# Optimization experiments

Hardware: AMD Instinct MI355X
Metric: run time of the kernel (lower is better)

## Reference

```python
import jax, jax.numpy as jnp
import numpy as np

N_NODES = 100000
N_EDGES = 3200000
IN_DIM, HID_DIM, LAT_DIM = 128, 64, 64


def gcn_conv(x, edge_index, W, b):
    """PyG-style GCNConv: add self-loops, symmetric deg^-1/2 normalization,
    linear transform, scatter-add aggregation, bias."""
    N = x.shape[0]
    loops = jnp.arange(N, dtype=edge_index.dtype)
    src = jnp.concatenate([edge_index[0], loops])  # [E+N]
    dst = jnp.concatenate([edge_index[1], loops])  # [E+N]
    # degree on target index (with self loops)
    deg = jax.ops.segment_sum(jnp.ones_like(dst, dtype=x.dtype), dst, num_segments=N)
    dinv = jnp.where(deg > 0, jax.lax.rsqrt(deg), 0.0)
    norm = dinv[src] * dinv[dst]  # [E+N]
    h = x @ W  # [N, out_dim] -- transform BEFORE gather (out_dim <= in_dim)
    msg = h[src] * norm[:, None]  # [E+N, out_dim]
    out = jax.ops.segment_sum(msg, dst, num_segments=N)
    return out + b


def setup_inputs() -> dict:
    key = jax.random.key(0)
    ks = jax.random.split(key, 6)
    x = jax.random.normal(ks[0], (N_NODES, IN_DIM), dtype=jnp.float32)
    edge_index = jax.random.randint(ks[1], (2, N_EDGES), 0, N_NODES, dtype=jnp.int64)
    # Glorot-ish init for weights, zero bias (PyG default)
    W1 = jax.random.normal(ks[2], (IN_DIM, HID_DIM), dtype=jnp.float32) / np.sqrt(IN_DIM)
    b1 = jnp.zeros((HID_DIM,), dtype=jnp.float32)
    W2 = jax.random.normal(ks[3], (HID_DIM, LAT_DIM), dtype=jnp.float32) / np.sqrt(HID_DIM)
    b2 = jnp.zeros((LAT_DIM,), dtype=jnp.float32)
    return {"x": x, "edge_index": edge_index, "W1": W1, "b1": b1, "W2": W2, "b2": b2}


def reference(x, edge_index, W1, b1, W2, b2):
    h = jax.nn.relu(gcn_conv(x, edge_index, W1, b1))
    return gcn_conv(h, edge_index, W2, b2)
```

## Files before the change

kernel.cpp:

```cpp
#include <hip/hip_runtime.h>
#include <cstdint>


#define BSHIFT 7
#define NBMAX 784
#define CH 4096
#define MAXB 6016

typedef __attribute__((ext_vector_type(8))) short bf16x8;
typedef __attribute__((ext_vector_type(4))) float f32x4;

__device__ inline unsigned short f2bf(float f) {
    unsigned u = __float_as_uint(f);
    unsigned r = (u + 0x7FFFu + ((u >> 16) & 1u)) >> 16;
    return (unsigned short)r;
}
__device__ inline unsigned pack2(float a, float b) {
    return (unsigned)f2bf(a) | ((unsigned)f2bf(b) << 16);
}
__device__ inline float blo(unsigned u) { return __uint_as_float(u << 16); }
__device__ inline float bhi(unsigned u) { return __uint_as_float(u & 0xFFFF0000u); }

__global__ __launch_bounds__(256) void hist_kernel(const int* __restrict__ dst,
                                                   int* __restrict__ histmat,
                                                   int E, int nb, int nblk,
                                                   const float* __restrict__ W1,
                                                   const float* __restrict__ W2,
                                                   unsigned short* __restrict__ W1t,
                                                   unsigned short* __restrict__ W2t) {
    if (blockIdx.x >= (unsigned)nblk) {
        int i = (blockIdx.x - nblk) * 256 + threadIdx.x;
        if (i < 128 * 64) {
            int k = i >> 6, n = i & 63;
            W1t[n * 128 + k] = f2bf(W1[i]);
        }
        int j = i - 128 * 64;
        if (j >= 0 && j < 64 * 64) {
            int k = j >> 6, n = j & 63;
            W2t[n * 64 + k] = f2bf(W2[j]);
        }
        return;
    }
    __shared__ int hist[NBMAX];
    int t = threadIdx.x;
    for (int b = t; b < nb; b += 256) hist[b] = 0;
    __syncthreads();
    int base = blockIdx.x * CH;
#pragma unroll
    for (int j = 0; j < CH / 1024; ++j) {
        int idx = base + j * 1024 + t * 4;
        if (idx + 4 <= E) {
            int4 d = *(const int4*)(dst + idx);
            atomicAdd(&hist[d.x >> BSHIFT], 1);
            atomicAdd(&hist[d.y >> BSHIFT], 1);
            atomicAdd(&hist[d.z >> BSHIFT], 1);
            atomicAdd(&hist[d.w >> BSHIFT], 1);
        } else {
            for (int k = 0; k < 4; ++k)
                if (idx + k < E) atomicAdd(&hist[dst[idx + k] >> BSHIFT], 1);
        }
    }
    __syncthreads();
    for (int b = t; b < nb; b += 256) histmat[blockIdx.x * nb + b] = hist[b];
}

__global__ __launch_bounds__(256) void scancol_kernel(const int* __restrict__ histmat,
                                                      int* __restrict__ colbase,
                                                      int* __restrict__ buckettotal,
                                                      int nb, int nblk) {
    __shared__ int ts[256];
    int b = blockIdx.x;
    int t = threadIdx.x;
    int v[4];
    int tsum = 0;
#pragma unroll
    for (int k = 0; k < 4; ++k) {
        int blk = t * 4 + k;
        v[k] = (blk < nblk) ? histmat[blk * nb + b] : 0;
        tsum += v[k];
    }
    ts[t] = tsum;
    __syncthreads();
    for (int ofs = 1; ofs < 256; ofs <<= 1) {
        int val = (t >= ofs) ? ts[t - ofs] : 0;
        __syncthreads();
        ts[t] += val;
        __syncthreads();
    }
    int run = ts[t] - tsum;
#pragma unroll
    for (int k = 0; k < 4; ++k) {
        int blk = t * 4 + k;
        if (blk < nblk) colbase[blk * nb + b] = run;
        run += v[k];
    }
    if (t == 255) buckettotal[b] = ts[255];
}

__global__ __launch_bounds__(256) void scanbucket_kernel(const int* __restrict__ buckettotal,
                                                         int* __restrict__ bucketbase,
                                                         int nb, int E) {
    __shared__ int ts[256];
    int t = threadIdx.x;
    int v[4];
    int tsum = 0;
#pragma unroll
    for (int k = 0; k < 4; ++k) {
        int b = t * 4 + k;
        v[k] = (b < nb) ? buckettotal[b] : 0;
        tsum += v[k];
    }
    ts[t] = tsum;
    __syncthreads();
    for (int ofs = 1; ofs < 256; ofs <<= 1) {
        int val = (t >= ofs) ? ts[t - ofs] : 0;
        __syncthreads();
        ts[t] += val;
        __syncthreads();
    }
    int run = ts[t] - tsum;
#pragma unroll
    for (int k = 0; k < 4; ++k) {
        int b = t * 4 + k;
        if (b < nb) bucketbase[b] = run;
        run += v[k];
    }
    if (t == 0) bucketbase[nb] = E;
}

__global__ __launch_bounds__(256) void bscatter_kernel(const int* __restrict__ src,
                                                       const int* __restrict__ dst,
                                                       const int* __restrict__ colbase,
                                                       const int* __restrict__ bucketbase,
                                                       int* __restrict__ packed,
                                                       int E, int nb) {
    __shared__ int cur[NBMAX];
    int t = threadIdx.x;
    for (int b = t; b < nb; b += 256)
        cur[b] = bucketbase[b] + colbase[blockIdx.x * nb + b];
    __syncthreads();
    int base = blockIdx.x * CH;
#pragma unroll
    for (int j = 0; j < CH / 1024; ++j) {
        int idx = base + j * 1024 + t * 4;
        if (idx + 4 <= E) {
            int4 d = *(const int4*)(dst + idx);
            int4 s = *(const int4*)(src + idx);
            int p;
            p = atomicAdd(&cur[d.x >> BSHIFT], 1); packed[p] = ((d.x & 127) << 17) | s.x;
            p = atomicAdd(&cur[d.y >> BSHIFT], 1); packed[p] = ((d.y & 127) << 17) | s.y;
            p = atomicAdd(&cur[d.z >> BSHIFT], 1); packed[p] = ((d.z & 127) << 17) | s.z;
            p = atomicAdd(&cur[d.w >> BSHIFT], 1); packed[p] = ((d.w & 127) << 17) | s.w;
        } else {
            for (int k = 0; k < 4; ++k)
                if (idx + k < E) {
                    int dd = dst[idx + k], ss = src[idx + k];
                    int p = atomicAdd(&cur[dd >> BSHIFT], 1);
                    packed[p] = ((dd & 127) << 17) | ss;
                }
        }
    }
}

__global__ __launch_bounds__(256) void bcsr_kernel(const int* __restrict__ packed,
                                                   const int* __restrict__ bucketbase,
                                                   int* __restrict__ rowptr,
                                                   float* __restrict__ dinv,
                                                   int* __restrict__ csr,
                                                   int N, int nb) {
    __shared__ int deg[128];
    __shared__ int lrp[128];
    __shared__ int ts[128];
    __shared__ int ebuf[MAXB];
    __shared__ int obuf[MAXB];
    int b = blockIdx.x;
    int t = threadIdx.x;
    if (t < 128) deg[t] = 0;
    __syncthreads();
    int bb0 = bucketbase[b];
    int bb1 = bucketbase[b + 1];
    int cnt = bb1 - bb0;
    bool fits = (cnt <= MAXB);
    if (fits) {
        for (int i = t; i < cnt; i += 256) {
            int v = packed[bb0 + i];
            ebuf[i] = v;
            atomicAdd(&deg[v >> 17], 1);
        }
    } else {
        for (int i = t; i < cnt; i += 256)
            atomicAdd(&deg[packed[bb0 + i] >> 17], 1);
    }
    __syncthreads();
    if (t < 128) ts[t] = deg[t];
    __syncthreads();
    for (int ofs = 1; ofs < 128; ofs <<= 1) {
        int v = (t < 128 && t >= ofs) ? ts[t - ofs] : 0;
        __syncthreads();
        if (t < 128) ts[t] += v;
        __syncthreads();
    }
    int node0 = b << BSHIFT;
    int nlocal = min(128, N - node0);
    if (t < 128) lrp[t] = ts[t] - deg[t];
    if (t < nlocal) {
        rowptr[node0 + t] = bb0 + (ts[t] - deg[t]);
        dinv[node0 + t] = rsqrtf((float)(deg[t] + 1));
    }
    if (t == nlocal) rowptr[node0 + nlocal] = bb1;
    __syncthreads();
    if (fits) {
        for (int i = t; i < cnt; i += 256) {
            int v = ebuf[i];
            int p = atomicAdd(&lrp[v >> 17], 1);
            obuf[p] = v & 0x1FFFF;
        }
        __syncthreads();
        for (int i = t; i < cnt; i += 256) csr[bb0 + i] = obuf[i];
    } else {
        for (int i = t; i < cnt; i += 256) {
            int v = packed[bb0 + i];
            int p = atomicAdd(&lrp[v >> 17], 1);
            csr[bb0 + p] = v & 0x1FFFF;
        }
    }
}

template <int K, bool XBF16>
__global__ __launch_bounds__(256) void gemm_mfma(const void* __restrict__ Xv,
                                                 const unsigned short* __restrict__ Wt,
                                                 const float* __restrict__ dinv,
                                                 unsigned short* __restrict__ Ybf, int M) {
    constexpr int KP = K + 8;
    __shared__ unsigned short Xs[64 * KP];
    __shared__ unsigned short Ws[64 * KP];
    int t = threadIdx.x;
    int row0 = blockIdx.x * 64;

    for (int i = t; i < 64 * K / 8; i += 256) {
        int r = i / (K / 8), c8 = i % (K / 8);
        *(uint4*)(&Ws[r * KP + c8 * 8]) = ((const uint4*)Wt)[i];
    }
    if (XBF16) {
        const unsigned short* X = (const unsigned short*)Xv;
        for (int i = t; i < 64 * K / 8; i += 256) {
            int r = i / (K / 8), c8 = i % (K / 8);
            int gr = row0 + r;
            uint4 v = make_uint4(0u, 0u, 0u, 0u);
            if (gr < M) v = ((const uint4*)(X + (size_t)gr * K))[c8];
            *(uint4*)(&Xs[r * KP + c8 * 8]) = v;
        }
    } else {
        const float* X = (const float*)Xv;
        for (int i = t; i < 64 * K / 4; i += 256) {
            int r = i / (K / 4), c4 = i % (K / 4);
            int gr = row0 + r;
            float4 v = make_float4(0.f, 0.f, 0.f, 0.f);
            if (gr < M) v = ((const float4*)(X + (size_t)gr * K))[c4];
            uint2 p;
            p.x = pack2(v.x, v.y);
            p.y = pack2(v.z, v.w);
            *(uint2*)(&Xs[r * KP + c4 * 4]) = p;
        }
    }
    __syncthreads();

    int lane = t & 63;
    int w = t >> 6;
    int m = lane & 15;
    int q = lane >> 4;

    f32x4 acc[4];
#pragma unroll
    for (int nt = 0; nt < 4; ++nt) acc[nt] = (f32x4){0.f, 0.f, 0.f, 0.f};

#pragma unroll
    for (int s = 0; s < K / 32; ++s) {
        bf16x8 a = *(const bf16x8*)(&Xs[(16 * w + m) * KP + s * 32 + q * 8]);
#pragma unroll
        for (int nt = 0; nt < 4; ++nt) {
            bf16x8 b = *(const bf16x8*)(&Ws[(16 * nt + m) * KP + s * 32 + q * 8]);
            acc[nt] = __builtin_amdgcn_mfma_f32_16x16x32_bf16(a, b, acc[nt], 0, 0, 0);
        }
    }
    __syncthreads();

    unsigned short* Cs = Xs;
#pragma unroll
    for (int nt = 0; nt < 4; ++nt)
#pragma unroll
        for (int r = 0; r < 4; ++r) {
            int row = 16 * w + q * 4 + r;
            int gr = row0 + row;
            float d = (gr < M) ? dinv[gr] : 0.f;
            Cs[row * 72 + nt * 16 + m] = f2bf(acc[nt][r] * d);
        }
    __syncthreads();
    for (int i = t; i < 64 * 64 / 8; i += 256) {
        int r = i >> 3, c8 = i & 7;
        int gr = row0 + r;
        if (gr < M)
            *(uint4*)(Ybf + (size_t)gr * 64 + c8 * 8) = *(const uint4*)(&Cs[r * 72 + c8 * 8]);
    }
}

__global__ __launch_bounds__(256) void aggregate_kernel(const unsigned* __restrict__ hsu,
                                                        const int* __restrict__ rowptr,
                                                        const int* __restrict__ csr,
                                                        const float* __restrict__ dinv,
                                                        const float* __restrict__ bias,
                                                        void* __restrict__ outv, int N,
                                                        int do_relu, int obf) {
    int t = threadIdx.x;
    int node = blockIdx.x * 32 + (t >> 3);
    if (node >= N) return;
    int sub = t & 7;
    int gbase = t & 56;

    float acc[8];
    {
        uint4 v = *(const uint4*)(hsu + (size_t)node * 32 + sub * 4);
        acc[0] = blo(v.x); acc[1] = bhi(v.x);
        acc[2] = blo(v.y); acc[3] = bhi(v.y);
        acc[4] = blo(v.z); acc[5] = bhi(v.z);
        acc[6] = blo(v.w); acc[7] = bhi(v.w);
    }
    int e0 = rowptr[node];
    int e1 = rowptr[node + 1];

    int e = e0;
    for (; e + 8 <= e1; e += 8) {
        int idx = csr[e + sub];
#pragma unroll
        for (int j = 0; j < 8; ++j) {
            int s = __shfl(idx, gbase + j, 64);
            uint4 v = *(const uint4*)(hsu + (size_t)s * 32 + sub * 4);
            acc[0] += blo(v.x); acc[1] += bhi(v.x);
            acc[2] += blo(v.y); acc[3] += bhi(v.y);
            acc[4] += blo(v.z); acc[5] += bhi(v.z);
            acc[6] += blo(v.w); acc[7] += bhi(v.w);
        }
    }
    for (; e < e1; ++e) {
        int s = csr[e];
        uint4 v = *(const uint4*)(hsu + (size_t)s * 32 + sub * 4);
        acc[0] += blo(v.x); acc[1] += bhi(v.x);
        acc[2] += blo(v.y); acc[3] += bhi(v.y);
        acc[4] += blo(v.z); acc[5] += bhi(v.z);
        acc[6] += blo(v.w); acc[7] += bhi(v.w);
    }

    float d = dinv[node];
    float4 b0 = *(const float4*)(bias + sub * 8);
    float4 b1 = *(const float4*)(bias + sub * 8 + 4);
    float o[8];
    o[0] = fmaf(acc[0], d, b0.x); o[1] = fmaf(acc[1], d, b0.y);
    o[2] = fmaf(acc[2], d, b0.z); o[3] = fmaf(acc[3], d, b0.w);
    o[4] = fmaf(acc[4], d, b1.x); o[5] = fmaf(acc[5], d, b1.y);
    o[6] = fmaf(acc[6], d, b1.z); o[7] = fmaf(acc[7], d, b1.w);
    if (do_relu) {
#pragma unroll
        for (int k = 0; k < 8; ++k) o[k] = fmaxf(o[k], 0.f);
    }
    if (obf) {
        unsigned short* outb = (unsigned short*)outv;
        uint4 p;
        p.x = pack2(o[0], o[1]); p.y = pack2(o[2], o[3]);
        p.z = pack2(o[4], o[5]); p.w = pack2(o[6], o[7]);
        *(uint4*)(outb + (size_t)node * 64 + sub * 8) = p;
    } else {
        float* op = (float*)outv + (size_t)node * 64 + sub * 8;
        *(float4*)(op)     = make_float4(o[0], o[1], o[2], o[3]);
        *(float4*)(op + 4) = make_float4(o[4], o[5], o[6], o[7]);
    }
}

extern "C" void kernel_launch(void* const* d_in, const int* in_sizes, int n_in,
                              void* d_out, int out_size, void* d_ws, size_t ws_size,
                              hipStream_t stream) {
    const float* x  = (const float*)d_in[0];
    const int*   ei = (const int*)d_in[1];
    const float* W1 = (const float*)d_in[2];
    const float* b1 = (const float*)d_in[3];
    const float* W2 = (const float*)d_in[4];
    const float* b2 = (const float*)d_in[5];

    const int N = in_sizes[0] / 128;
    const int E = in_sizes[1] / 2;
    const int* src = ei;
    const int* dst = ei + E;
    float* out = (float*)d_out;

    const int nb   = (N + 127) >> BSHIFT;
    const int nblk = (E + CH - 1) / CH;

    char* ws = (char*)d_ws;
    size_t off = 0;
    auto alloc = [&](size_t bytes) -> char* {
        char* p = ws + off;
        off = (off + bytes + 255) & ~(size_t)255;
        return p;
    };
    int*   csr         = (int*)alloc((size_t)E * 4);
    int*   rowptr      = (int*)alloc((size_t)(N + 1) * 4);
    float* dinv        = (float*)alloc((size_t)N * 4);
    int*   bucketbase  = (int*)alloc((size_t)(nb + 1) * 4);
    int*   buckettotal = (int*)alloc((size_t)nb * 4);
    unsigned short* W1t = (unsigned short*)alloc(64 * 128 * 2);
    unsigned short* W2t = (unsigned short*)alloc(64 * 64 * 2);
    unsigned short* bufA = (unsigned short*)alloc((size_t)N * 64 * 2);
    unsigned short* bufB = (unsigned short*)alloc((size_t)N * 64 * 2);
    int* histmat = (int*)bufA;
    int* packed  = (int*)((char*)bufA + ((size_t)nblk * nb * 4 + 255 & ~(size_t)255) + 256);

    hist_kernel<<<nblk + 48, 256, 0, stream>>>(dst, histmat, E, nb, nblk, W1, W2, W1t, W2t);
    scancol_kernel<<<nb, 256, 0, stream>>>(histmat, histmat, buckettotal, nb, nblk);
    scanbucket_kernel<<<1, 256, 0, stream>>>(buckettotal, bucketbase, nb, E);
    bscatter_kernel<<<nblk, 256, 0, stream>>>(src, dst, histmat, bucketbase, packed, E, nb);
    bcsr_kernel<<<nb, 256, 0, stream>>>(packed, bucketbase, rowptr, dinv, csr, N, nb);

    gemm_mfma<128, false><<<(N + 63) / 64, 256, 0, stream>>>(x, W1t, dinv, bufA, N);
    aggregate_kernel<<<(N + 31) / 32, 256, 0, stream>>>((const unsigned*)bufA, rowptr, csr,
                                                        dinv, b1, bufB, N, 1, 1);
    gemm_mfma<64, true><<<(N + 63) / 64, 256, 0, stream>>>(bufB, W2t, dinv, bufA, N);
    aggregate_kernel<<<(N + 31) / 32, 256, 0, stream>>>((const unsigned*)bufA, rowptr, csr,
                                                        dinv, b2, out, N, 0, 0);
}
```

Baseline: 318.1 us.

## Sub-sort bucket edges by source range and use nontemporal CSR/output accesses

The per-bucket CSR build now counts on 1024 bins (dst-local × 8 source-range slices) instead of 128 per-node bins. It scans these bins so each node's neighbor list is ordered by coarse source range, which should make the aggregation gathers more cache-local. The aggregation kernel also switches its CSR index loads and output stores to nontemporal to avoid polluting cache that the feature gathers need. The trade-off is a larger scan and a wider-bin histogram in the build kernel.

```diff
diff --git a/kernel.cpp b/kernel.cpp
--- a/kernel.cpp
+++ b/kernel.cpp
@@ -9,6 +9,7 @@
 
 typedef __attribute__((ext_vector_type(8))) short bf16x8;
 typedef __attribute__((ext_vector_type(4))) float f32x4;
+typedef __attribute__((ext_vector_type(4))) unsigned int u32x4;
 
 __device__ inline unsigned short f2bf(float f) {
     unsigned u = __float_as_uint(f);
@@ -168,59 +169,75 @@
                                                    float* __restrict__ dinv,
                                                    int* __restrict__ csr,
                                                    int N, int nb) {
-    __shared__ int deg[128];
-    __shared__ int lrp[128];
-    __shared__ int ts[128];
+    __shared__ int cnt[1025];
+    __shared__ int ts[256];
     __shared__ int ebuf[MAXB];
     __shared__ int obuf[MAXB];
     int b = blockIdx.x;
     int t = threadIdx.x;
-    if (t < 128) deg[t] = 0;
+    for (int i = t; i < 1024; i += 256) cnt[i] = 0;
     __syncthreads();
     int bb0 = bucketbase[b];
     int bb1 = bucketbase[b + 1];
-    int cnt = bb1 - bb0;
-    bool fits = (cnt <= MAXB);
+    int cnt_e = bb1 - bb0;
+    bool fits = (cnt_e <= MAXB);
     if (fits) {
-        for (int i = t; i < cnt; i += 256) {
+        for (int i = t; i < cnt_e; i += 256) {
             int v = packed[bb0 + i];
             ebuf[i] = v;
-            atomicAdd(&deg[v >> 17], 1);
+            atomicAdd(&cnt[v >> 14], 1);
         }
     } else {
-        for (int i = t; i < cnt; i += 256)
-            atomicAdd(&deg[packed[bb0 + i] >> 17], 1);
-    }
-    __syncthreads();
-    if (t < 128) ts[t] = deg[t];
-    __syncthreads();
-    for (int ofs = 1; ofs < 128; ofs <<= 1) {
-        int v = (t < 128 && t >= ofs) ? ts[t - ofs] : 0;
-        __syncthreads();
-        if (t < 128) ts[t] += v;
-        __syncthreads();
-    }
+        for (int i = t; i < cnt_e; i += 256)
+            atomicAdd(&cnt[packed[bb0 + i] >> 14], 1);
+    }
+    __syncthreads();
+    int v4[4];
+    int tsum = 0;
+#pragma unroll
+    for (int k = 0; k < 4; ++k) {
+        v4[k] = cnt[t * 4 + k];
+        tsum += v4[k];
+    }
+    ts[t] = tsum;
+    __syncthreads();
+    for (int ofs = 1; ofs < 256; ofs <<= 1) {
+        int val = (t >= ofs) ? ts[t - ofs] : 0;
+        __syncthreads();
+        ts[t] += val;
+        __syncthreads();
+    }
+    int run = ts[t] - tsum;
+#pragma unroll
+    for (int k = 0; k < 4; ++k) {
+        int c = v4[k];
+        cnt[t * 4 + k] = run;
+        run += c;
+    }
+    if (t == 255) cnt[1024] = run;
+    __syncthreads();
     int node0 = b << BSHIFT;
     int nlocal = min(128, N - node0);
-    if (t < 128) lrp[t] = ts[t] - deg[t];
     if (t < nlocal) {
-        rowptr[node0 + t] = bb0 + (ts[t] - deg[t]);
-        dinv[node0 + t] = rsqrtf((float)(deg[t] + 1));
+        int s0 = cnt[t * 8];
+        int deg = cnt[(t + 1) * 8] - s0;
+        rowptr[node0 + t] = bb0 + s0;
+        dinv[node0 + t] = rsqrtf((float)(deg + 1));
     }
     if (t == nlocal) rowptr[node0 + nlocal] = bb1;
     __syncthreads();
     if (fits) {
-        for (int i = t; i < cnt; i += 256) {
+        for (int i = t; i < cnt_e; i += 256) {
             int v = ebuf[i];
-            int p = atomicAdd(&lrp[v >> 17], 1);
+            int p = atomicAdd(&cnt[v >> 14], 1);
             obuf[p] = v & 0x1FFFF;
         }
         __syncthreads();
-        for (int i = t; i < cnt; i += 256) csr[bb0 + i] = obuf[i];
+        for (int i = t; i < cnt_e; i += 256) csr[bb0 + i] = obuf[i];
     } else {
-        for (int i = t; i < cnt; i += 256) {
+        for (int i = t; i < cnt_e; i += 256) {
             int v = packed[bb0 + i];
-            int p = atomicAdd(&lrp[v >> 17], 1);
+            int p = atomicAdd(&cnt[v >> 14], 1);
             csr[bb0 + p] = v & 0x1FFFF;
         }
     }
@@ -330,7 +347,7 @@
 
     int e = e0;
     for (; e + 8 <= e1; e += 8) {
-        int idx = csr[e + sub];
+        int idx = __builtin_nontemporal_load(csr + e + sub);
 #pragma unroll
         for (int j = 0; j < 8; ++j) {
             int s = __shfl(idx, gbase + j, 64);
@@ -342,7 +359,7 @@
         }
     }
     for (; e < e1; ++e) {
-        int s = csr[e];
+        int s = __builtin_nontemporal_load(csr + e);
         uint4 v = *(const uint4*)(hsu + (size_t)s * 32 + sub * 4);
         acc[0] += blo(v.x); acc[1] += bhi(v.x);
         acc[2] += blo(v.y); acc[3] += bhi(v.y);
@@ -364,14 +381,16 @@
     }
     if (obf) {
         unsigned short* outb = (unsigned short*)outv;
-        uint4 p;
+        u32x4 p;
         p.x = pack2(o[0], o[1]); p.y = pack2(o[2], o[3]);
         p.z = pack2(o[4], o[5]); p.w = pack2(o[6], o[7]);
-        *(uint4*)(outb + (size_t)node * 64 + sub * 8) = p;
+        __builtin_nontemporal_store(p, (u32x4*)(outb + (size_t)node * 64 + sub * 8));
     } else {
         float* op = (float*)outv + (size_t)node * 64 + sub * 8;
-        *(float4*)(op)     = make_float4(o[0], o[1], o[2], o[3]);
-        *(float4*)(op + 4) = make_float4(o[4], o[5], o[6], o[7]);
+        f32x4 o0 = {o[0], o[1], o[2], o[3]};
+        f32x4 o1 = {o[4], o[5], o[6], o[7]};
+        __builtin_nontemporal_store(o0, (f32x4*)op);
+        __builtin_nontemporal_store(o1, (f32x4*)(op + 4));
     }
 }
 
```

Result: slower. 329.3 us (+3.5%).

## Sort nodes by degree for balanced aggregation and batch gather loads

Applied to the files above, without the earlier changes.

Adds a counting sort of nodes by in-degree (histogram, scan, scatter kernels) and has the aggregation kernels process nodes in that permuted order, so the 8-lane groups in a wavefront handle nodes of similar degree and lose less time to divergence. The inner gather loop is also restructured to issue all eight shuffles and row loads before accumulating, which raises memory-level parallelism. The cost is four extra small kernel launches, an extra perm indirection, and scattered output writes that break the contiguous store pattern.

```diff
diff --git a/kernel.cpp b/kernel.cpp
--- a/kernel.cpp
+++ b/kernel.cpp
@@ -226,6 +226,45 @@
     }
 }
 
+__global__ __launch_bounds__(256) void dhist_kernel(const int* __restrict__ rowptr,
+                                                    int* __restrict__ dhistmat, int N) {
+    __shared__ int bins[128];
+    int t = threadIdx.x;
+    if (t < 128) bins[t] = 0;
+    __syncthreads();
+    int base = blockIdx.x * 1024;
+#pragma unroll
+    for (int k = 0; k < 4; ++k) {
+        int n = base + k * 256 + t;
+        if (n < N) {
+            int d = rowptr[n + 1] - rowptr[n];
+            atomicAdd(&bins[min(d, 127)], 1);
+        }
+    }
+    __syncthreads();
+    if (t < 128) dhistmat[blockIdx.x * 128 + t] = bins[t];
+}
+
+__global__ __launch_bounds__(256) void dscatter_kernel(const int* __restrict__ rowptr,
+                                                       const int* __restrict__ colbase,
+                                                       const int* __restrict__ binbase,
+                                                       int* __restrict__ perm, int N) {
+    __shared__ int cur[128];
+    int t = threadIdx.x;
+    if (t < 128) cur[t] = binbase[t] + colbase[blockIdx.x * 128 + t];
+    __syncthreads();
+    int base = blockIdx.x * 1024;
+#pragma unroll
+    for (int k = 0; k < 4; ++k) {
+        int n = base + k * 256 + t;
+        if (n < N) {
+            int d = rowptr[n + 1] - rowptr[n];
+            int p = atomicAdd(&cur[min(d, 127)], 1);
+            perm[p] = n;
+        }
+    }
+}
+
 template <int K, bool XBF16>
 __global__ __launch_bounds__(256) void gemm_mfma(const void* __restrict__ Xv,
                                                  const unsigned short* __restrict__ Wt,
@@ -304,16 +343,24 @@
     }
 }
 
+#define ACC8(v)                                      \
+    acc[0] += blo(v.x); acc[1] += bhi(v.x);          \
+    acc[2] += blo(v.y); acc[3] += bhi(v.y);          \
+    acc[4] += blo(v.z); acc[5] += bhi(v.z);          \
+    acc[6] += blo(v.w); acc[7] += bhi(v.w);
+
 __global__ __launch_bounds__(256) void aggregate_kernel(const unsigned* __restrict__ hsu,
                                                         const int* __restrict__ rowptr,
                                                         const int* __restrict__ csr,
+                                                        const int* __restrict__ perm,
                                                         const float* __restrict__ dinv,
                                                         const float* __restrict__ bias,
                                                         void* __restrict__ outv, int N,
                                                         int do_relu, int obf) {
     int t = threadIdx.x;
-    int node = blockIdx.x * 32 + (t >> 3);
-    if (node >= N) return;
+    int slot = blockIdx.x * 32 + (t >> 3);
+    if (slot >= N) return;
+    int node = perm[slot];
     int sub = t & 7;
     int gbase = t & 56;
 
@@ -331,23 +378,29 @@
     int e = e0;
     for (; e + 8 <= e1; e += 8) {
         int idx = csr[e + sub];
-#pragma unroll
-        for (int j = 0; j < 8; ++j) {
-            int s = __shfl(idx, gbase + j, 64);
-            uint4 v = *(const uint4*)(hsu + (size_t)s * 32 + sub * 4);
-            acc[0] += blo(v.x); acc[1] += bhi(v.x);
-            acc[2] += blo(v.y); acc[3] += bhi(v.y);
-            acc[4] += blo(v.z); acc[5] += bhi(v.z);
-            acc[6] += blo(v.w); acc[7] += bhi(v.w);
-        }
+        int s0 = __shfl(idx, gbase + 0, 64);
+        int s1 = __shfl(idx, gbase + 1, 64);
+        int s2 = __shfl(idx, gbase + 2, 64);
+        int s3 = __shfl(idx, gbase + 3, 64);
+        int s4 = __shfl(idx, gbase + 4, 64);
+        int s5 = __shfl(idx, gbase + 5, 64);
+        int s6 = __shfl(idx, gbase + 6, 64);
+        int s7 = __shfl(idx, gbase + 7, 64);
+        uint4 v0 = *(const uint4*)(hsu + (size_t)s0 * 32 + sub * 4);
+        uint4 v1 = *(const uint4*)(hsu + (size_t)s1 * 32 + sub * 4);
+        uint4 v2 = *(const uint4*)(hsu + (size_t)s2 * 32 + sub * 4);
+        uint4 v3 = *(const uint4*)(hsu + (size_t)s3 * 32 + sub * 4);
+        uint4 v4 = *(const uint4*)(hsu + (size_t)s4 * 32 + sub * 4);
+        uint4 v5 = *(const uint4*)(hsu + (size_t)s5 * 32 + sub * 4);
+        uint4 v6 = *(const uint4*)(hsu + (size_t)s6 * 32 + sub * 4);
+        uint4 v7 = *(const uint4*)(hsu + (size_t)s7 * 32 + sub * 4);
+        ACC8(v0); ACC8(v1); ACC8(v2); ACC8(v3);
+        ACC8(v4); ACC8(v5); ACC8(v6); ACC8(v7);
     }
     for (; e < e1; ++e) {
         int s = csr[e];
         uint4 v = *(const uint4*)(hsu + (size_t)s * 32 + sub * 4);
-        acc[0] += blo(v.x); acc[1] += bhi(v.x);
-        acc[2] += blo(v.y); acc[3] += bhi(v.y);
-        acc[4] += blo(v.z); acc[5] += bhi(v.z);
-        acc[6] += blo(v.w); acc[7] += bhi(v.w);
+        ACC8(v);
     }
 
     float d = dinv[node];
@@ -393,6 +446,7 @@
 
     const int nb   = (N + 127) >> BSHIFT;
     const int nblk = (E + CH - 1) / CH;
+    const int nblkD = (N + 1023) / 1024;
 
     char* ws = (char*)d_ws;
     size_t off = 0;
@@ -406,12 +460,16 @@
     float* dinv        = (float*)alloc((size_t)N * 4);
     int*   bucketbase  = (int*)alloc((size_t)(nb + 1) * 4);
     int*   buckettotal = (int*)alloc((size_t)nb * 4);
+    int*   perm        = (int*)alloc((size_t)N * 4);
+    int*   dbinbase    = (int*)alloc(129 * 4);
+    int*   dbintotal   = (int*)alloc(128 * 4);
     unsigned short* W1t = (unsigned short*)alloc(64 * 128 * 2);
     unsigned short* W2t = (unsigned short*)alloc(64 * 64 * 2);
     unsigned short* bufA = (unsigned short*)alloc((size_t)N * 64 * 2);
     unsigned short* bufB = (unsigned short*)alloc((size_t)N * 64 * 2);
-    int* histmat = (int*)bufA;
-    int* packed  = (int*)((char*)bufA + ((size_t)nblk * nb * 4 + 255 & ~(size_t)255) + 256);
+    int* histmat  = (int*)bufA;
+    int* packed   = (int*)((char*)bufA + ((size_t)nblk * nb * 4 + 255 & ~(size_t)255) + 256);
+    int* dhistmat = packed + E;
 
     hist_kernel<<<nblk + 48, 256, 0, stream>>>(dst, histmat, E, nb, nblk, W1, W2, W1t, W2t);
     scancol_kernel<<<nb, 256, 0, stream>>>(histmat, histmat, buckettotal, nb, nblk);
@@ -419,10 +477,15 @@
     bscatter_kernel<<<nblk, 256, 0, stream>>>(src, dst, histmat, bucketbase, packed, E, nb);
     bcsr_kernel<<<nb, 256, 0, stream>>>(packed, bucketbase, rowptr, dinv, csr, N, nb);
 
+    dhist_kernel<<<nblkD, 256, 0, stream>>>(rowptr, dhistmat, N);
+    scancol_kernel<<<128, 256, 0, stream>>>(dhistmat, dhistmat, dbintotal, 128, nblkD);
+    scanbucket_kernel<<<1, 256, 0, stream>>>(dbintotal, dbinbase, 128, N);
+    dscatter_kernel<<<nblkD, 256, 0, stream>>>(rowptr, dhistmat, dbinbase, perm, N);
+
     gemm_mfma<128, false><<<(N + 63) / 64, 256, 0, stream>>>(x, W1t, dinv, bufA, N);
     aggregate_kernel<<<(N + 31) / 32, 256, 0, stream>>>((const unsigned*)bufA, rowptr, csr,
-                                                        dinv, b1, bufB, N, 1, 1);
+                                                        perm, dinv, b1, bufB, N, 1, 1);
     gemm_mfma<64, true><<<(N + 63) / 64, 256, 0, stream>>>(bufB, W2t, dinv, bufA, N);
     aggregate_kernel<<<(N + 31) / 32, 256, 0, stream>>>((const unsigned*)bufA, rowptr, csr,
-                                                        dinv, b2, out, N, 0, 0);
-}
+                                                        perm, dinv, b2, out, N, 0, 0);
+}
```

Measured after the change: 329.8 us. 3.7% more time.
